# Performance work log

Measured on AMD Instinct MI355X. Metric: run time of the kernel, lower is better.

The kernel has to match this reference:

```python
import jax, jax.numpy as jnp
import numpy as np

N_NODES = 100_000
SCALAR_DIM = 64
HIDDEN = 64
ATTR_DIM = 3
N_DIH = 1_000_000
IN_DIM = SCALAR_DIM * 2 + ATTR_DIM + 2  # 133
EPS_LN = 1e-5
EPS_NORM = 1e-6


def setup_inputs() -> dict:
    key = jax.random.key(0)
    ks = jax.random.split(key, 8)
    x = jax.random.normal(ks[0], (N_NODES, SCALAR_DIM), jnp.float32)
    pos = jax.random.normal(ks[1], (N_NODES, 3), jnp.float32)
    quadra_index = jax.random.randint(ks[2], (4, N_DIH), 0, N_NODES, jnp.int32)
    quadra_attr = jax.random.normal(ks[3], (N_DIH, ATTR_DIM), jnp.float32)

    def lin(k, fi, fo):
        lim = 1.0 / np.sqrt(fi)
        return jax.random.uniform(k, (fi, fo), jnp.float32, -lim, lim)

    return dict(
        x=x, pos=pos, quadra_index=quadra_index, quadra_attr=quadra_attr,
        ln_gamma=jnp.ones((IN_DIM,), jnp.float32),
        ln_beta=jnp.zeros((IN_DIM,), jnp.float32),
        w1=lin(ks[4], IN_DIM, HIDDEN), b1=jnp.zeros((HIDDEN,), jnp.float32),
        w2=lin(ks[5], HIDDEN, HIDDEN), b2=jnp.zeros((HIDDEN,), jnp.float32),
        w3=lin(ks[6], HIDDEN, SCALAR_DIM), b3=jnp.zeros((SCALAR_DIM,), jnp.float32),
        w_out=jax.random.normal(ks[7], (SCALAR_DIM, SCALAR_DIM), jnp.float32),
    )


def _dihedral_cos_sin(pos, i, j, k, l):
    b1 = pos[j] - pos[i]
    b2 = pos[k] - pos[j]
    b3 = pos[l] - pos[k]
    n1 = jnp.cross(b1, b2)
    n2 = jnp.cross(b2, b3)
    n1 = n1 / jnp.maximum(jnp.linalg.norm(n1, axis=-1, keepdims=True), EPS_NORM)
    n2 = n2 / jnp.maximum(jnp.linalg.norm(n2, axis=-1, keepdims=True), EPS_NORM)
    cos_d = jnp.clip(jnp.sum(n1 * n2, axis=-1), -1.0, 1.0)
    b2n = b2 / jnp.maximum(jnp.linalg.norm(b2, axis=-1, keepdims=True), EPS_NORM)
    m = jnp.cross(n1, b2n)
    sin_d = jnp.sum(m * n2, axis=-1)
    return cos_d, sin_d


def _segment_mean(v, idx, n):
    s = jax.ops.segment_sum(v, idx, num_segments=n)
    c = jax.ops.segment_sum(jnp.ones((idx.shape[0], 1), v.dtype), idx, num_segments=n)
    return s / jnp.maximum(c, 1.0)


def reference(x, pos, quadra_index, quadra_attr,
              ln_gamma, ln_beta, w1, b1, w2, b2, w3, b3, w_out):
    i, j, k, l = quadra_index[0], quadra_index[1], quadra_index[2], quadra_index[3]
    x_scalar = x[:, :SCALAR_DIM]
    cos_d, sin_d = _dihedral_cos_sin(pos, i, j, k, l)
    # [num_dihedrals, 2*scalar_dim + 3 + 2]
    inp = jnp.concatenate(
        [x_scalar[i], x_scalar[l], quadra_attr, cos_d[:, None], sin_d[:, None]], axis=-1)
    # LayerNorm over last dim
    mu = jnp.mean(inp, axis=-1, keepdims=True)
    var = jnp.mean(jnp.square(inp - mu), axis=-1, keepdims=True)
    inp = (inp - mu) * jax.lax.rsqrt(var + EPS_LN) * ln_gamma + ln_beta
    # MLP with SiLU
    h = jax.nn.silu(inp @ w1 + b1)
    h = jax.nn.silu(h @ w2 + b2)
    msg = h @ w3 + b3  # [num_dihedrals, scalar_dim]
    aggr = 0.5 * (_segment_mean(msg, j, N_NODES) + _segment_mean(msg, k, N_NODES))
    # e3nn o3.Linear on scalars: fan-in normalized linear, no bias
    out = (aggr @ w_out) * (1.0 / np.sqrt(SCALAR_DIM))
    return out
```

## Files before the change

### kernel.cpp

```cpp
#include <hip/hip_runtime.h>
#include <math.h>

#define NN 100000
#define ND 1000000
#define INDIM 133
#define K1P 160
#define NCNT (2*NN)
#define SCAN_CHUNK 2048
#define NBLK_SCAN ((NCNT + SCAN_CHUNK - 1) / SCAN_CHUNK)
#define HS 72

typedef __bf16 bf16x8 __attribute__((ext_vector_type(8)));
typedef __bf16 bf16x4 __attribute__((ext_vector_type(4)));
typedef float  f32x4  __attribute__((ext_vector_type(4)));
typedef _Float16 f16;
typedef _Float16 f16x4 __attribute__((ext_vector_type(4)));

__device__ __forceinline__ f32x4 mfma_bf16(bf16x8 a, bf16x8 b, f32x4 c) {
    return __builtin_amdgcn_mfma_f32_16x16x32_bf16(a, b, c, 0, 0, 0);
}

__device__ __forceinline__ float3 f3sub(float3 a, float3 b) {
    return make_float3(a.x - b.x, a.y - b.y, a.z - b.z);
}
__device__ __forceinline__ float3 f3cross(float3 a, float3 b) {
    return make_float3(a.y * b.z - a.z * b.y, a.z * b.x - a.x * b.z, a.x * b.y - a.y * b.x);
}
__device__ __forceinline__ float f3dot(float3 a, float3 b) {
    return a.x * b.x + a.y * b.y + a.z * b.z;
}
__device__ __forceinline__ float3 f3load(const float* __restrict__ p, int idx) {
    const float* q = p + (size_t)idx * 3;
    return make_float3(q[0], q[1], q[2]);
}
__device__ __forceinline__ float fsilu(float v) {
    return v / (1.0f + __expf(-v));
}

__global__ __launch_bounds__(256) void prep_w1g(const float* __restrict__ w1,
                                                const float* __restrict__ gamma,
                                                __bf16* __restrict__ hi,
                                                __bf16* __restrict__ lo) {
    int idx = blockIdx.x * 256 + threadIdx.x;
    if (idx >= 64 * K1P) return;
    int n = idx / K1P, kp = idx - n * K1P;
    float v = (kp < INDIM) ? gamma[kp] * w1[(size_t)kp * 64 + n] : 0.0f;
    __bf16 h = (__bf16)v;
    hi[idx] = h;
    lo[idx] = (__bf16)(v - (float)h);
}

__global__ __launch_bounds__(64) void prep_lin(const float* __restrict__ w1,
                                               const float* __restrict__ b1,
                                               const float* __restrict__ gamma,
                                               const float* __restrict__ beta,
                                               float* __restrict__ c1,
                                               float* __restrict__ d1) {
    const int c = threadIdx.x;
    float sc = 0.0f, sd = 0.0f;
    for (int k = 0; k < INDIM; ++k) {
        float w = w1[(size_t)k * 64 + c];
        sc = fmaf(gamma[k], w, sc);
        sd = fmaf(beta[k], w, sd);
    }
    c1[c] = sc;
    d1[c] = sd + b1[c];
}

__global__ __launch_bounds__(256) void prep_w(const float* __restrict__ w,
                                              __bf16* __restrict__ hi,
                                              __bf16* __restrict__ lo) {
    int idx = blockIdx.x * 256 + threadIdx.x;
    if (idx >= 64 * 64) return;
    int n = idx >> 6, kp = idx & 63;
    int ko = 16 * (kp & 3) + (kp >> 2);
    float v = w[(size_t)ko * 64 + n];
    __bf16 h = (__bf16)v;
    hi[idx] = h;
    lo[idx] = (__bf16)(v - (float)h);
}

__global__ __launch_bounds__(256) void prep_w3(const float* __restrict__ w3,
                                               const float* __restrict__ b3,
                                               const float* __restrict__ wout,
                                               __bf16* __restrict__ hiT,
                                               __bf16* __restrict__ loT,
                                               float* __restrict__ b3f) {
    const int tid = threadIdx.x;
    for (int idx = tid; idx < 64 * 64; idx += 256) {
        int k = idx >> 6, c = idx & 63;
        float s = 0.0f;
        for (int q = 0; q < 64; ++q)
            s = fmaf(w3[(size_t)k * 64 + q], wout[(size_t)q * 64 + c], s);
        s *= 0.0625f;
        __bf16 h = (__bf16)s;
        int kp = 4 * (k & 15) + (k >> 4);
        hiT[(size_t)c * 64 + kp] = h;
        loT[(size_t)c * 64 + kp] = (__bf16)(s - (float)h);
    }
    if (tid < 64) {
        float s = 0.0f;
        for (int q = 0; q < 64; ++q)
            s = fmaf(b3[q], wout[(size_t)q * 64 + tid], s);
        b3f[tid] = s * 0.0625f;
    }
}

__global__ __launch_bounds__(256) void count_kernel(const int* __restrict__ qidx,
                                                    int* __restrict__ cnt) {
    int e = blockIdx.x * 256 + threadIdx.x;
    if (e < ND) {
        atomicAdd(&cnt[qidx[ND + e]], 1);
        atomicAdd(&cnt[NN + qidx[2 * ND + e]], 1);
    }
}

__global__ __launch_bounds__(256) void scan1(int* data, int* __restrict__ bsum) {
    __shared__ int lds[256];
    const int tid = threadIdx.x;
    const int base = blockIdx.x * SCAN_CHUNK + tid * 8;
    int v[8];
    int tsum = 0;
#pragma unroll
    for (int t = 0; t < 8; ++t) {
        v[t] = (base + t < NCNT) ? data[base + t] : 0;
        tsum += v[t];
    }
    lds[tid] = tsum;
    __syncthreads();
    for (int d = 1; d < 256; d <<= 1) {
        int t = 0;
        if (tid >= d) t = lds[tid - d];
        __syncthreads();
        lds[tid] += t;
        __syncthreads();
    }
    if (tid == 255) bsum[blockIdx.x] = lds[255];
    int run = lds[tid] - tsum;
#pragma unroll
    for (int t = 0; t < 8; ++t) {
        if (base + t < NCNT) data[base + t] = run;
        run += v[t];
    }
}

__global__ __launch_bounds__(128) void scan2(int* __restrict__ bsum) {
    __shared__ int lds[128];
    const int t = threadIdx.x;
    int v = (t < NBLK_SCAN) ? bsum[t] : 0;
    lds[t] = v;
    __syncthreads();
    for (int d = 1; d < 128; d <<= 1) {
        int u = (t >= d) ? lds[t - d] : 0;
        __syncthreads();
        lds[t] += u;
        __syncthreads();
    }
    if (t < NBLK_SCAN) bsum[t] = lds[t] - v;
}

__global__ __launch_bounds__(256) void scan3(int* __restrict__ off,
                                             const int* __restrict__ bsum) {
    const int base = blockIdx.x * SCAN_CHUNK + threadIdx.x * 8;
    const int add = bsum[blockIdx.x];
#pragma unroll
    for (int t = 0; t < 8; ++t) {
        int i = base + t;
        if (i < NCNT) off[i] += add;
    }
}

__global__ __launch_bounds__(256) void fill_kernel(const int* __restrict__ qidx,
                                                   int* __restrict__ off,
                                                   int* __restrict__ slot_j,
                                                   int* __restrict__ slot_k) {
    int e = blockIdx.x * 256 + threadIdx.x;
    if (e < ND) {
        slot_j[e] = atomicAdd(&off[qidx[ND + e]], 1);
        slot_k[e] = atomicAdd(&off[NN + qidx[2 * ND + e]], 1);
    }
}

__global__ __launch_bounds__(256, 3) void edge_mlp_mfma(
    const float* __restrict__ x, const float* __restrict__ pos,
    const int* __restrict__ qidx, const float* __restrict__ qattr,
    const __bf16* __restrict__ w1h, const __bf16* __restrict__ w1l,
    const float* __restrict__ c1, const float* __restrict__ d1,
    const __bf16* __restrict__ w2h, const __bf16* __restrict__ w2l, const float* __restrict__ b2,
    const __bf16* __restrict__ w3h, const __bf16* __restrict__ w3l, const float* __restrict__ b3f,
    const int* __restrict__ slot_j, const int* __restrict__ slot_k,
    f16* __restrict__ msg)
{
    __shared__ __align__(16) __bf16 hsh[4][2][16 * HS];

    const int tid = threadIdx.x;
    const int w   = tid >> 6;
    const int l   = tid & 63;
    const int m   = l & 15;
    const int kg  = l >> 4;
    const int ebase = (blockIdx.x * 4 + w) * 32;
    if (ebase >= ND) return;

    int iA[2], lA[2];
#pragma unroll
    for (int t = 0; t < 2; ++t) {
        const int e = ebase + 16 * t + m;
        iA[t] = qidx[e];
        lA[t] = qidx[3 * ND + e];
    }

    float cosd = 0.f, sind = 0.f, at0 = 0.f, at1 = 0.f, at2 = 0.f, se = 0.f, qe = 0.f;
    if (kg < 2) {
        const int e2 = ebase + 16 * kg + m;
        const int j2 = qidx[ND + e2];
        const int k2 = qidx[2 * ND + e2];
        float3 pi = f3load(pos, iA[kg]), pj = f3load(pos, j2);
        float3 pk = f3load(pos, k2), pl = f3load(pos, lA[kg]);
        float3 d1v_ = f3sub(pj, pi);
        float3 d2v_ = f3sub(pk, pj);
        float3 d3v_ = f3sub(pl, pk);
        float3 n1 = f3cross(d1v_, d2v_);
        float3 n2 = f3cross(d2v_, d3v_);
        float r1 = 1.0f / fmaxf(sqrtf(f3dot(n1, n1)), 1e-6f);
        n1.x *= r1; n1.y *= r1; n1.z *= r1;
        float r2 = 1.0f / fmaxf(sqrtf(f3dot(n2, n2)), 1e-6f);
        n2.x *= r2; n2.y *= r2; n2.z *= r2;
        cosd = fminf(fmaxf(f3dot(n1, n2), -1.0f), 1.0f);
        float rb = 1.0f / fmaxf(sqrtf(f3dot(d2v_, d2v_)), 1e-6f);
        float3 b2n = make_float3(d2v_.x * rb, d2v_.y * rb, d2v_.z * rb);
        float3 mm = f3cross(n1, b2n);
        sind = f3dot(mm, n2);
        at0 = qattr[(size_t)e2 * 3 + 0];
        at1 = qattr[(size_t)e2 * 3 + 1];
        at2 = qattr[(size_t)e2 * 3 + 2];
        se = at0 + at1 + at2 + cosd + sind;
        qe = at0 * at0 + at1 * at1 + at2 * at2 + cosd * cosd + sind * sind;
    }

    bf16x8 ah4[2], al4[2];
#pragma unroll
    for (int t = 0; t < 2; ++t) {
        const int src = m + 16 * t;
        float u4[8] = {__shfl(at0, src), __shfl(at1, src), __shfl(at2, src),
                       __shfl(cosd, src), __shfl(sind, src), 0.f, 0.f, 0.f};
        float g0 = (kg == 0) ? 1.0f : 0.0f;
#pragma unroll
        for (int j = 0; j < 8; ++j) {
            float v = u4[j] * g0;
            __bf16 h = (__bf16)v;
            ah4[t][j] = h;
            al4[t][j] = (__bf16)(v - (float)h);
        }
    }

    f32x4 acc[2][4];
#pragma unroll
    for (int t = 0; t < 2; ++t)
#pragma unroll
        for (int nt = 0; nt < 4; ++nt) acc[t][nt] = (f32x4){0.f, 0.f, 0.f, 0.f};

#pragma unroll
    for (int nt = 0; nt < 4; ++nt) {
        const size_t wb = (size_t)(16 * nt + m) * K1P + 128 + 8 * kg;
        bf16x8 bh = *(const bf16x8*)(w1h + wb);
        bf16x8 bl = *(const bf16x8*)(w1l + wb);
        acc[0][nt] = mfma_bf16(ah4[0], bh, acc[0][nt]);
        acc[0][nt] = mfma_bf16(al4[0], bh, acc[0][nt]);
        acc[0][nt] = mfma_bf16(ah4[0], bl, acc[0][nt]);
        acc[1][nt] = mfma_bf16(ah4[1], bh, acc[1][nt]);
        acc[1][nt] = mfma_bf16(al4[1], bh, acc[1][nt]);
        acc[1][nt] = mfma_bf16(ah4[1], bl, acc[1][nt]);
    }

    float st1[2] = {0.f, 0.f}, st2[2] = {0.f, 0.f};
#pragma unroll
    for (int s = 0; s < 4; ++s) {
        const int r0 = (s < 2) ? iA[0] : lA[0];
        const int r1 = (s < 2) ? iA[1] : lA[1];
        const int colo = 32 * (s & 1) + 8 * kg;
        float vv0[8], vv1[8];
        *(float4*)&vv0[0] = *(const float4*)(x + (size_t)r0 * 64 + colo);
        *(float4*)&vv0[4] = *(const float4*)(x + (size_t)r0 * 64 + colo + 4);
        *(float4*)&vv1[0] = *(const float4*)(x + (size_t)r1 * 64 + colo);
        *(float4*)&vv1[4] = *(const float4*)(x + (size_t)r1 * 64 + colo + 4);
        bf16x8 a0h, a0l, a1h, a1l;
#pragma unroll
        for (int j = 0; j < 8; ++j) {
            float v0 = vv0[j], v1 = vv1[j];
            __bf16 h0 = (__bf16)v0, h1 = (__bf16)v1;
            a0h[j] = h0; a0l[j] = (__bf16)(v0 - (float)h0);
            a1h[j] = h1; a1l[j] = (__bf16)(v1 - (float)h1);
            st1[0] += v0; st2[0] = fmaf(v0, v0, st2[0]);
            st1[1] += v1; st2[1] = fmaf(v1, v1, st2[1]);
        }
#pragma unroll
        for (int nt = 0; nt < 4; ++nt) {
            const size_t wb = (size_t)(16 * nt + m) * K1P + 32 * s + 8 * kg;
            bf16x8 bh = *(const bf16x8*)(w1h + wb);
            bf16x8 bl = *(const bf16x8*)(w1l + wb);
            acc[0][nt] = mfma_bf16(a0h, bh, acc[0][nt]);
            acc[0][nt] = mfma_bf16(a0l, bh, acc[0][nt]);
            acc[0][nt] = mfma_bf16(a0h, bl, acc[0][nt]);
            acc[1][nt] = mfma_bf16(a1h, bh, acc[1][nt]);
            acc[1][nt] = mfma_bf16(a1l, bh, acc[1][nt]);
            acc[1][nt] = mfma_bf16(a1h, bl, acc[1][nt]);
        }
    }

    float rs_[2], mn_[2];
#pragma unroll
    for (int t = 0; t < 2; ++t) {
        float s1 = st1[t], s2 = st2[t];
        s1 += __shfl_xor(s1, 16); s1 += __shfl_xor(s1, 32);
        s2 += __shfl_xor(s2, 16); s2 += __shfl_xor(s2, 32);
        const int src = m + 16 * t;
        float S = s1 + __shfl(se, src);
        float Q = s2 + __shfl(qe, src);
        float mu  = S * (1.0f / INDIM);
        float var = Q * (1.0f / INDIM) - mu * mu;
        float rsv = rsqrtf(fmaxf(var, 0.0f) + 1e-5f);
        rs_[t] = rsv;
        mn_[t] = -mu * rsv;
    }

    float c1v[4], d1v[4], b2v[4], b3v[4];
#pragma unroll
    for (int nt = 0; nt < 4; ++nt) {
        c1v[nt] = c1[16 * nt + m];
        d1v[nt] = d1[16 * nt + m];
        b2v[nt] = b2[16 * nt + m];
        b3v[nt] = b3f[16 * nt + m];
    }
#pragma unroll
    for (int t = 0; t < 2; ++t) {
        __bf16* hhw = &hsh[w][t][0];
#pragma unroll
        for (int r = 0; r < 4; ++r) {
            float rse = __shfl(rs_[t], 4 * kg + r);
            float mne = __shfl(mn_[t], 4 * kg + r);
            bf16x4 hv4;
#pragma unroll
            for (int nt = 0; nt < 4; ++nt)
                hv4[nt] = (__bf16)fsilu(fmaf(rse, acc[t][nt][r],
                                        fmaf(mne, c1v[nt], d1v[nt])));
            *(bf16x4*)(hhw + (4 * kg + r) * HS + m * 4) = hv4;
        }
    }

    bf16x8 a2h[2][2];
#pragma unroll
    for (int t = 0; t < 2; ++t)
#pragma unroll
        for (int s = 0; s < 2; ++s)
            a2h[t][s] = *(const bf16x8*)(&hsh[w][t][m * HS + 32 * s + 8 * kg]);
    f32x4 acc2[2][4];
#pragma unroll
    for (int t = 0; t < 2; ++t)
#pragma unroll
        for (int nt = 0; nt < 4; ++nt) acc2[t][nt] = (f32x4){0.f, 0.f, 0.f, 0.f};
#pragma unroll
    for (int s = 0; s < 2; ++s) {
#pragma unroll
        for (int nt = 0; nt < 4; ++nt) {
            const size_t wb = (size_t)(16 * nt + m) * 64 + 32 * s + 8 * kg;
            bf16x8 bh = *(const bf16x8*)(w2h + wb);
            bf16x8 bl = *(const bf16x8*)(w2l + wb);
            acc2[0][nt] = mfma_bf16(a2h[0][s], bh, acc2[0][nt]);
            acc2[0][nt] = mfma_bf16(a2h[0][s], bl, acc2[0][nt]);
            acc2[1][nt] = mfma_bf16(a2h[1][s], bh, acc2[1][nt]);
            acc2[1][nt] = mfma_bf16(a2h[1][s], bl, acc2[1][nt]);
        }
    }
#pragma unroll
    for (int t = 0; t < 2; ++t) {
        __bf16* hhw = &hsh[w][t][0];
#pragma unroll
        for (int r = 0; r < 4; ++r) {
            bf16x4 hv4;
#pragma unroll
            for (int nt = 0; nt < 4; ++nt)
                hv4[nt] = (__bf16)fsilu(acc2[t][nt][r] + b2v[nt]);
            *(bf16x4*)(hhw + (4 * kg + r) * HS + m * 4) = hv4;
        }
    }

    bf16x8 a3h[2][2];
#pragma unroll
    for (int t = 0; t < 2; ++t)
#pragma unroll
        for (int s = 0; s < 2; ++s)
            a3h[t][s] = *(const bf16x8*)(&hsh[w][t][m * HS + 32 * s + 8 * kg]);
    f32x4 acc3[2][4];
#pragma unroll
    for (int t = 0; t < 2; ++t)
#pragma unroll
        for (int nt = 0; nt < 4; ++nt) acc3[t][nt] = (f32x4){0.f, 0.f, 0.f, 0.f};
#pragma unroll
    for (int s = 0; s < 2; ++s) {
#pragma unroll
        for (int nt = 0; nt < 4; ++nt) {
            const size_t wb = (size_t)(16 * nt + m) * 64 + 32 * s + 8 * kg;
            bf16x8 bh = *(const bf16x8*)(w3h + wb);
            bf16x8 bl = *(const bf16x8*)(w3l + wb);
            acc3[0][nt] = mfma_bf16(a3h[0][s], bh, acc3[0][nt]);
            acc3[0][nt] = mfma_bf16(a3h[0][s], bl, acc3[0][nt]);
            acc3[1][nt] = mfma_bf16(a3h[1][s], bh, acc3[1][nt]);
            acc3[1][nt] = mfma_bf16(a3h[1][s], bl, acc3[1][nt]);
        }
    }

#pragma unroll
    for (int t = 0; t < 2; ++t) {
#pragma unroll
        for (int r = 0; r < 4; ++r) {
            f16x4 v;
#pragma unroll
            for (int nt = 0; nt < 4; ++nt)
                v[nt] = (f16)(acc3[t][nt][r] + b3v[nt]);
            const int er = ebase + 16 * t + 4 * kg + r;
            *(f16x4*)(msg + (size_t)slot_j[er] * 64 + m * 4) = v;
            *(f16x4*)(msg + (size_t)slot_k[er] * 64 + m * 4) = v;
        }
    }
}

__global__ __launch_bounds__(256) void node_out(const f16* __restrict__ msg,
                                                const int* __restrict__ off,
                                                float* __restrict__ out) {
    const int w   = threadIdx.x >> 6;
    const int l   = threadIdx.x & 63;
    const int sub = l >> 4;
    const int m16 = l & 15;
    for (int n = blockIdx.x * 4 + w; n < NN; n += gridDim.x * 4) {
        int ja = (n == 0) ? 0 : off[n - 1];
        int jb = off[n];
        int ka = off[NN + n - 1];
        int kb = off[NN + n];
        float s0 = 0.f, s1 = 0.f, s2 = 0.f, s3 = 0.f;
        float t0 = 0.f, t1 = 0.f, t2 = 0.f, t3 = 0.f;
        for (int p = ja + sub; p < jb; p += 4) {
            f16x4 v = *(const f16x4*)(msg + (size_t)p * 64 + m16 * 4);
            s0 += (float)v[0]; s1 += (float)v[1];
            s2 += (float)v[2]; s3 += (float)v[3];
        }
        for (int p = ka + sub; p < kb; p += 4) {
            f16x4 v = *(const f16x4*)(msg + (size_t)p * 64 + m16 * 4);
            t0 += (float)v[0]; t1 += (float)v[1];
            t2 += (float)v[2]; t3 += (float)v[3];
        }
        s0 += __shfl_xor(s0, 16); s0 += __shfl_xor(s0, 32);
        s1 += __shfl_xor(s1, 16); s1 += __shfl_xor(s1, 32);
        s2 += __shfl_xor(s2, 16); s2 += __shfl_xor(s2, 32);
        s3 += __shfl_xor(s3, 16); s3 += __shfl_xor(s3, 32);
        t0 += __shfl_xor(t0, 16); t0 += __shfl_xor(t0, 32);
        t1 += __shfl_xor(t1, 16); t1 += __shfl_xor(t1, 32);
        t2 += __shfl_xor(t2, 16); t2 += __shfl_xor(t2, 32);
        t3 += __shfl_xor(t3, 16); t3 += __shfl_xor(t3, 32);
        if (sub == 0) {
            float rj = 1.0f / fmaxf((float)(jb - ja), 1.0f);
            float rk = 1.0f / fmaxf((float)(kb - ka), 1.0f);
            float* o = out + (size_t)n * 64;
            o[m16]      = s0 * rj + t0 * rk;
            o[16 + m16] = s1 * rj + t1 * rk;
            o[32 + m16] = s2 * rj + t2 * rk;
            o[48 + m16] = s3 * rj + t3 * rk;
        }
    }
}


extern "C" void kernel_launch(void* const* d_in, const int* in_sizes, int n_in,
                              void* d_out, int out_size, void* d_ws, size_t ws_size,
                              hipStream_t stream) {
    (void)in_sizes; (void)n_in; (void)out_size;

    const float* x     = (const float*)d_in[0];
    const float* pos   = (const float*)d_in[1];
    const int*   qidx  = (const int*)d_in[2];
    const float* qattr = (const float*)d_in[3];
    const float* gamma = (const float*)d_in[4];
    const float* beta  = (const float*)d_in[5];
    const float* w1    = (const float*)d_in[6];
    const float* b1    = (const float*)d_in[7];
    const float* w2    = (const float*)d_in[8];
    const float* b2    = (const float*)d_in[9];
    const float* w3    = (const float*)d_in[10];
    const float* b3    = (const float*)d_in[11];
    const float* w_out = (const float*)d_in[12];
    float* out = (float*)d_out;

    size_t o = 0;
    auto alloc = [&](size_t bytes) { size_t r = o; o = (o + bytes + 255) & ~(size_t)255; return r; };
    char* W = (char*)d_ws;
    f16*    msg    = (f16*)   (W + alloc((size_t)2 * ND * 64 * sizeof(f16)));
    int*    slot_j = (int*)   (W + alloc((size_t)ND * sizeof(int)));
    int*    slot_k = (int*)   (W + alloc((size_t)ND * sizeof(int)));
    int*    off    = (int*)   (W + alloc((size_t)NCNT * sizeof(int)));
    int*    bsum   = (int*)   (W + alloc((size_t)NBLK_SCAN * sizeof(int)));
    __bf16* w1h    = (__bf16*)(W + alloc((size_t)64 * K1P * sizeof(__bf16)));
    __bf16* w1l    = (__bf16*)(W + alloc((size_t)64 * K1P * sizeof(__bf16)));
    __bf16* w2h    = (__bf16*)(W + alloc((size_t)64 * 64 * sizeof(__bf16)));
    __bf16* w2l    = (__bf16*)(W + alloc((size_t)64 * 64 * sizeof(__bf16)));
    __bf16* w3h    = (__bf16*)(W + alloc((size_t)64 * 64 * sizeof(__bf16)));
    __bf16* w3l    = (__bf16*)(W + alloc((size_t)64 * 64 * sizeof(__bf16)));
    float*  c1     = (float*) (W + alloc((size_t)64 * sizeof(float)));
    float*  d1     = (float*) (W + alloc((size_t)64 * sizeof(float)));
    float*  b3f    = (float*) (W + alloc((size_t)64 * sizeof(float)));
    if (ws_size < o) return;

    prep_w1g<<<(64 * K1P + 255) / 256, 256, 0, stream>>>(w1, gamma, w1h, w1l);
    prep_lin<<<1, 64, 0, stream>>>(w1, b1, gamma, beta, c1, d1);
    prep_w<<<16, 256, 0, stream>>>(w2, w2h, w2l);
    prep_w3<<<1, 256, 0, stream>>>(w3, b3, w_out, w3h, w3l, b3f);

    hipMemsetAsync(off, 0, (size_t)NCNT * sizeof(int), stream);
    count_kernel<<<(ND + 255) / 256, 256, 0, stream>>>(qidx, off);
    scan1<<<NBLK_SCAN, 256, 0, stream>>>(off, bsum);
    scan2<<<1, 128, 0, stream>>>(bsum);
    scan3<<<NBLK_SCAN, 256, 0, stream>>>(off, bsum);
    fill_kernel<<<(ND + 255) / 256, 256, 0, stream>>>(qidx, off, slot_j, slot_k);

    edge_mlp_mfma<<<(ND + 127) / 128, 256, 0, stream>>>(x, pos, qidx, qattr,
                                                        w1h, w1l, c1, d1,
                                                        w2h, w2l, b2, w3h, w3l, b3f,
                                                        slot_j, slot_k, msg);
    node_out<<<4096, 256, 0, stream>>>(msg, off, out);
}
```

Baseline: 595.9 us.

## Process 64 edges per wave, precompute per-node LN stats, merge prep kernels

Each wave in the edge MLP now handles 64 dihedrals instead of 32, so every loaded bf16 weight fragment is reused across four row tiles, and all four lane groups now do dihedral geometry instead of two. Per-node sum and sum-of-squares of x are precomputed once by a new kernel, so LayerNorm statistics become two float2 gathers instead of an in-kernel reduction. The four weight-prep kernels are merged into one launch. In exchange, the accumulator count doubles, which raises register pressure and may reduce occupancy under the 3-blocks-per-SM bound, and LDS use grows.

```diff
diff --git a/kernel.cpp b/kernel.cpp
--- a/kernel.cpp
+++ b/kernel.cpp
@@ -37,72 +37,77 @@
     return v / (1.0f + __expf(-v));
 }
 
-__global__ __launch_bounds__(256) void prep_w1g(const float* __restrict__ w1,
-                                                const float* __restrict__ gamma,
-                                                __bf16* __restrict__ hi,
-                                                __bf16* __restrict__ lo) {
-    int idx = blockIdx.x * 256 + threadIdx.x;
-    if (idx >= 64 * K1P) return;
-    int n = idx / K1P, kp = idx - n * K1P;
-    float v = (kp < INDIM) ? gamma[kp] * w1[(size_t)kp * 64 + n] : 0.0f;
-    __bf16 h = (__bf16)v;
-    hi[idx] = h;
-    lo[idx] = (__bf16)(v - (float)h);
-}
-
-__global__ __launch_bounds__(64) void prep_lin(const float* __restrict__ w1,
-                                               const float* __restrict__ b1,
-                                               const float* __restrict__ gamma,
-                                               const float* __restrict__ beta,
-                                               float* __restrict__ c1,
-                                               float* __restrict__ d1) {
-    const int c = threadIdx.x;
-    float sc = 0.0f, sd = 0.0f;
-    for (int k = 0; k < INDIM; ++k) {
-        float w = w1[(size_t)k * 64 + c];
-        sc = fmaf(gamma[k], w, sc);
-        sd = fmaf(beta[k], w, sd);
-    }
-    c1[c] = sc;
-    d1[c] = sd + b1[c];
-}
-
-__global__ __launch_bounds__(256) void prep_w(const float* __restrict__ w,
-                                              __bf16* __restrict__ hi,
-                                              __bf16* __restrict__ lo) {
-    int idx = blockIdx.x * 256 + threadIdx.x;
-    if (idx >= 64 * 64) return;
-    int n = idx >> 6, kp = idx & 63;
-    int ko = 16 * (kp & 3) + (kp >> 2);
-    float v = w[(size_t)ko * 64 + n];
-    __bf16 h = (__bf16)v;
-    hi[idx] = h;
-    lo[idx] = (__bf16)(v - (float)h);
-}
-
-__global__ __launch_bounds__(256) void prep_w3(const float* __restrict__ w3,
-                                               const float* __restrict__ b3,
-                                               const float* __restrict__ wout,
-                                               __bf16* __restrict__ hiT,
-                                               __bf16* __restrict__ loT,
-                                               float* __restrict__ b3f) {
-    const int tid = threadIdx.x;
-    for (int idx = tid; idx < 64 * 64; idx += 256) {
-        int k = idx >> 6, c = idx & 63;
-        float s = 0.0f;
-        for (int q = 0; q < 64; ++q)
-            s = fmaf(w3[(size_t)k * 64 + q], wout[(size_t)q * 64 + c], s);
-        s *= 0.0625f;
-        __bf16 h = (__bf16)s;
-        int kp = 4 * (k & 15) + (k >> 4);
-        hiT[(size_t)c * 64 + kp] = h;
-        loT[(size_t)c * 64 + kp] = (__bf16)(s - (float)h);
-    }
-    if (tid < 64) {
-        float s = 0.0f;
-        for (int q = 0; q < 64; ++q)
-            s = fmaf(b3[q], wout[(size_t)q * 64 + tid], s);
-        b3f[tid] = s * 0.0625f;
+__global__ __launch_bounds__(256) void prep_sq(const float* __restrict__ x,
+                                               float2* __restrict__ sq) {
+    const int n = blockIdx.x * 4 + (threadIdx.x >> 6);
+    const int c = threadIdx.x & 63;
+    float v = x[(size_t)n * 64 + c];
+    float s = v, q = v * v;
+#pragma unroll
+    for (int d = 1; d < 64; d <<= 1) {
+        s += __shfl_xor(s, d);
+        q += __shfl_xor(q, d);
+    }
+    if (c == 0) sq[n] = make_float2(s, q);
+}
+
+__global__ __launch_bounds__(256) void prep_all(
+    const float* __restrict__ w1, const float* __restrict__ b1,
+    const float* __restrict__ w2,
+    const float* __restrict__ w3, const float* __restrict__ b3,
+    const float* __restrict__ wout,
+    const float* __restrict__ gamma, const float* __restrict__ beta,
+    __bf16* __restrict__ w1h, __bf16* __restrict__ w1l,
+    float* __restrict__ c1, float* __restrict__ d1,
+    __bf16* __restrict__ w2h, __bf16* __restrict__ w2l,
+    __bf16* __restrict__ w3h, __bf16* __restrict__ w3l,
+    float* __restrict__ b3f)
+{
+    const int b = blockIdx.x, tid = threadIdx.x;
+    if (b < 40) {
+        int idx = b * 256 + tid;
+        int n = idx / K1P, kp = idx - n * K1P;
+        float v = (kp < INDIM) ? gamma[kp] * w1[(size_t)kp * 64 + n] : 0.0f;
+        __bf16 h = (__bf16)v;
+        w1h[idx] = h;
+        w1l[idx] = (__bf16)(v - (float)h);
+    } else if (b == 40) {
+        if (tid < 64) {
+            float sc = 0.0f, sd = 0.0f;
+            for (int k = 0; k < INDIM; ++k) {
+                float wv = w1[(size_t)k * 64 + tid];
+                sc = fmaf(gamma[k], wv, sc);
+                sd = fmaf(beta[k], wv, sd);
+            }
+            c1[tid] = sc;
+            d1[tid] = sd + b1[tid];
+        }
+    } else if (b < 57) {
+        int idx = (b - 41) * 256 + tid;
+        int n = idx >> 6, kp = idx & 63;
+        int ko = 16 * (kp & 3) + (kp >> 2);
+        float v = w2[(size_t)ko * 64 + n];
+        __bf16 h = (__bf16)v;
+        w2h[idx] = h;
+        w2l[idx] = (__bf16)(v - (float)h);
+    } else {
+        for (int idx = tid; idx < 64 * 64; idx += 256) {
+            int k = idx >> 6, c = idx & 63;
+            float s = 0.0f;
+            for (int q = 0; q < 64; ++q)
+                s = fmaf(w3[(size_t)k * 64 + q], wout[(size_t)q * 64 + c], s);
+            s *= 0.0625f;
+            __bf16 h = (__bf16)s;
+            int kp = 4 * (k & 15) + (k >> 4);
+            w3h[(size_t)c * 64 + kp] = h;
+            w3l[(size_t)c * 64 + kp] = (__bf16)(s - (float)h);
+        }
+        if (tid < 64) {
+            float s = 0.0f;
+            for (int q = 0; q < 64; ++q)
+                s = fmaf(b3[q], wout[(size_t)q * 64 + tid], s);
+            b3f[tid] = s * 0.0625f;
+        }
     }
 }
 
@@ -182,7 +187,8 @@
 }
 
 __global__ __launch_bounds__(256, 3) void edge_mlp_mfma(
-    const float* __restrict__ x, const float* __restrict__ pos,
+    const float* __restrict__ x, const float2* __restrict__ sq,
+    const float* __restrict__ pos,
     const int* __restrict__ qidx, const float* __restrict__ qattr,
     const __bf16* __restrict__ w1h, const __bf16* __restrict__ w1l,
     const float* __restrict__ c1, const float* __restrict__ d1,
@@ -191,31 +197,33 @@
     const int* __restrict__ slot_j, const int* __restrict__ slot_k,
     f16* __restrict__ msg)
 {
-    __shared__ __align__(16) __bf16 hsh[4][2][16 * HS];
+    __shared__ __align__(16) __bf16 hsh[4][4][16 * HS];
 
     const int tid = threadIdx.x;
     const int w   = tid >> 6;
     const int l   = tid & 63;
     const int m   = l & 15;
     const int kg  = l >> 4;
-    const int ebase = (blockIdx.x * 4 + w) * 32;
+    const int ebase = (blockIdx.x * 4 + w) * 64;
     if (ebase >= ND) return;
 
-    int iA[2], lA[2];
-#pragma unroll
-    for (int t = 0; t < 2; ++t) {
+    int iA[4], lA[4];
+#pragma unroll
+    for (int t = 0; t < 4; ++t) {
         const int e = ebase + 16 * t + m;
         iA[t] = qidx[e];
         lA[t] = qidx[3 * ND + e];
     }
 
-    float cosd = 0.f, sind = 0.f, at0 = 0.f, at1 = 0.f, at2 = 0.f, se = 0.f, qe = 0.f;
-    if (kg < 2) {
+    float cosd, sind, at0, at1, at2, se, qe;
+    {
         const int e2 = ebase + 16 * kg + m;
+        const int i2 = qidx[e2];
         const int j2 = qidx[ND + e2];
         const int k2 = qidx[2 * ND + e2];
-        float3 pi = f3load(pos, iA[kg]), pj = f3load(pos, j2);
-        float3 pk = f3load(pos, k2), pl = f3load(pos, lA[kg]);
+        const int l2 = qidx[3 * ND + e2];
+        float3 pi = f3load(pos, i2), pj = f3load(pos, j2);
+        float3 pk = f3load(pos, k2), pl = f3load(pos, l2);
         float3 d1v_ = f3sub(pj, pi);
         float3 d2v_ = f3sub(pk, pj);
         float3 d3v_ = f3sub(pl, pk);
@@ -237,9 +245,10 @@
         qe = at0 * at0 + at1 * at1 + at2 * at2 + cosd * cosd + sind * sind;
     }
 
-    bf16x8 ah4[2], al4[2];
-#pragma unroll
-    for (int t = 0; t < 2; ++t) {
+    bf16x8 ah4[4], al4[4];
+    float rs_[4], mn_[4];
+#pragma unroll
+    for (int t = 0; t < 4; ++t) {
         const int src = m + 16 * t;
         float u4[8] = {__shfl(at0, src), __shfl(at1, src), __shfl(at2, src),
                        __shfl(cosd, src), __shfl(sind, src), 0.f, 0.f, 0.f};
@@ -251,71 +260,9 @@
             ah4[t][j] = h;
             al4[t][j] = (__bf16)(v - (float)h);
         }
-    }
-
-    f32x4 acc[2][4];
-#pragma unroll
-    for (int t = 0; t < 2; ++t)
-#pragma unroll
-        for (int nt = 0; nt < 4; ++nt) acc[t][nt] = (f32x4){0.f, 0.f, 0.f, 0.f};
-
-#pragma unroll
-    for (int nt = 0; nt < 4; ++nt) {
-        const size_t wb = (size_t)(16 * nt + m) * K1P + 128 + 8 * kg;
-        bf16x8 bh = *(const bf16x8*)(w1h + wb);
-        bf16x8 bl = *(const bf16x8*)(w1l + wb);
-        acc[0][nt] = mfma_bf16(ah4[0], bh, acc[0][nt]);
-        acc[0][nt] = mfma_bf16(al4[0], bh, acc[0][nt]);
-        acc[0][nt] = mfma_bf16(ah4[0], bl, acc[0][nt]);
-        acc[1][nt] = mfma_bf16(ah4[1], bh, acc[1][nt]);
-        acc[1][nt] = mfma_bf16(al4[1], bh, acc[1][nt]);
-        acc[1][nt] = mfma_bf16(ah4[1], bl, acc[1][nt]);
-    }
-
-    float st1[2] = {0.f, 0.f}, st2[2] = {0.f, 0.f};
-#pragma unroll
-    for (int s = 0; s < 4; ++s) {
-        const int r0 = (s < 2) ? iA[0] : lA[0];
-        const int r1 = (s < 2) ? iA[1] : lA[1];
-        const int colo = 32 * (s & 1) + 8 * kg;
-        float vv0[8], vv1[8];
-        *(float4*)&vv0[0] = *(const float4*)(x + (size_t)r0 * 64 + colo);
-        *(float4*)&vv0[4] = *(const float4*)(x + (size_t)r0 * 64 + colo + 4);
-        *(float4*)&vv1[0] = *(const float4*)(x + (size_t)r1 * 64 + colo);
-        *(float4*)&vv1[4] = *(const float4*)(x + (size_t)r1 * 64 + colo + 4);
-        bf16x8 a0h, a0l, a1h, a1l;
-#pragma unroll
-        for (int j = 0; j < 8; ++j) {
-            float v0 = vv0[j], v1 = vv1[j];
-            __bf16 h0 = (__bf16)v0, h1 = (__bf16)v1;
-            a0h[j] = h0; a0l[j] = (__bf16)(v0 - (float)h0);
-            a1h[j] = h1; a1l[j] = (__bf16)(v1 - (float)h1);
-            st1[0] += v0; st2[0] = fmaf(v0, v0, st2[0]);
-            st1[1] += v1; st2[1] = fmaf(v1, v1, st2[1]);
-        }
-#pragma unroll
-        for (int nt = 0; nt < 4; ++nt) {
-            const size_t wb = (size_t)(16 * nt + m) * K1P + 32 * s + 8 * kg;
-            bf16x8 bh = *(const bf16x8*)(w1h + wb);
-            bf16x8 bl = *(const bf16x8*)(w1l + wb);
-            acc[0][nt] = mfma_bf16(a0h, bh, acc[0][nt]);
-            acc[0][nt] = mfma_bf16(a0l, bh, acc[0][nt]);
-            acc[0][nt] = mfma_bf16(a0h, bl, acc[0][nt]);
-            acc[1][nt] = mfma_bf16(a1h, bh, acc[1][nt]);
-            acc[1][nt] = mfma_bf16(a1l, bh, acc[1][nt]);
-            acc[1][nt] = mfma_bf16(a1h, bl, acc[1][nt]);
-        }
-    }
-
-    float rs_[2], mn_[2];
-#pragma unroll
-    for (int t = 0; t < 2; ++t) {
-        float s1 = st1[t], s2 = st2[t];
-        s1 += __shfl_xor(s1, 16); s1 += __shfl_xor(s1, 32);
-        s2 += __shfl_xor(s2, 16); s2 += __shfl_xor(s2, 32);
-        const int src = m + 16 * t;
-        float S = s1 + __shfl(se, src);
-        float Q = s2 + __shfl(qe, src);
+        float2 si = sq[iA[t]], sl = sq[lA[t]];
+        float S = si.x + sl.x + __shfl(se, src);
+        float Q = si.y + sl.y + __shfl(qe, src);
         float mu  = S * (1.0f / INDIM);
         float var = Q * (1.0f / INDIM) - mu * mu;
         float rsv = rsqrtf(fmaxf(var, 0.0f) + 1e-5f);
@@ -323,6 +270,57 @@
         mn_[t] = -mu * rsv;
     }
 
+    f32x4 acc[4][4];
+#pragma unroll
+    for (int t = 0; t < 4; ++t)
+#pragma unroll
+        for (int nt = 0; nt < 4; ++nt) acc[t][nt] = (f32x4){0.f, 0.f, 0.f, 0.f};
+
+#pragma unroll
+    for (int nt = 0; nt < 4; ++nt) {
+        const size_t wb = (size_t)(16 * nt + m) * K1P + 128 + 8 * kg;
+        bf16x8 bh = *(const bf16x8*)(w1h + wb);
+        bf16x8 bl = *(const bf16x8*)(w1l + wb);
+#pragma unroll
+        for (int t = 0; t < 4; ++t) {
+            acc[t][nt] = mfma_bf16(ah4[t], bh, acc[t][nt]);
+            acc[t][nt] = mfma_bf16(al4[t], bh, acc[t][nt]);
+            acc[t][nt] = mfma_bf16(ah4[t], bl, acc[t][nt]);
+        }
+    }
+
+#pragma unroll
+    for (int s = 0; s < 4; ++s) {
+        const int colo = 32 * (s & 1) + 8 * kg;
+        bf16x8 ath[4], atl[4];
+#pragma unroll
+        for (int t = 0; t < 4; ++t) {
+            const int r_ = (s < 2) ? iA[t] : lA[t];
+            float vv[8];
+            *(float4*)&vv[0] = *(const float4*)(x + (size_t)r_ * 64 + colo);
+            *(float4*)&vv[4] = *(const float4*)(x + (size_t)r_ * 64 + colo + 4);
+#pragma unroll
+            for (int j = 0; j < 8; ++j) {
+                float v = vv[j];
+                __bf16 h = (__bf16)v;
+                ath[t][j] = h;
+                atl[t][j] = (__bf16)(v - (float)h);
+            }
+        }
+#pragma unroll
+        for (int nt = 0; nt < 4; ++nt) {
+            const size_t wb = (size_t)(16 * nt + m) * K1P + 32 * s + 8 * kg;
+            bf16x8 bh = *(const bf16x8*)(w1h + wb);
+            bf16x8 bl = *(const bf16x8*)(w1l + wb);
+#pragma unroll
+            for (int t = 0; t < 4; ++t) {
+                acc[t][nt] = mfma_bf16(ath[t], bh, acc[t][nt]);
+                acc[t][nt] = mfma_bf16(atl[t], bh, acc[t][nt]);
+                acc[t][nt] = mfma_bf16(ath[t], bl, acc[t][nt]);
+            }
+        }
+    }
+
     float c1v[4], d1v[4], b2v[4], b3v[4];
 #pragma unroll
     for (int nt = 0; nt < 4; ++nt) {
@@ -332,7 +330,7 @@
         b3v[nt] = b3f[16 * nt + m];
     }
 #pragma unroll
-    for (int t = 0; t < 2; ++t) {
+    for (int t = 0; t < 4; ++t) {
         __bf16* hhw = &hsh[w][t][0];
 #pragma unroll
         for (int r = 0; r < 4; ++r) {
@@ -347,15 +345,15 @@
         }
     }
 
-    bf16x8 a2h[2][2];
-#pragma unroll
-    for (int t = 0; t < 2; ++t)
+    bf16x8 a2h[4][2];
+#pragma unroll
+    for (int t = 0; t < 4; ++t)
 #pragma unroll
         for (int s = 0; s < 2; ++s)
             a2h[t][s] = *(const bf16x8*)(&hsh[w][t][m * HS + 32 * s + 8 * kg]);
-    f32x4 acc2[2][4];
-#pragma unroll
-    for (int t = 0; t < 2; ++t)
+    f32x4 acc2[4][4];
+#pragma unroll
+    for (int t = 0; t < 4; ++t)
 #pragma unroll
         for (int nt = 0; nt < 4; ++nt) acc2[t][nt] = (f32x4){0.f, 0.f, 0.f, 0.f};
 #pragma unroll
@@ -365,14 +363,15 @@
             const size_t wb = (size_t)(16 * nt + m) * 64 + 32 * s + 8 * kg;
             bf16x8 bh = *(const bf16x8*)(w2h + wb);
             bf16x8 bl = *(const bf16x8*)(w2l + wb);
-            acc2[0][nt] = mfma_bf16(a2h[0][s], bh, acc2[0][nt]);
-            acc2[0][nt] = mfma_bf16(a2h[0][s], bl, acc2[0][nt]);
-            acc2[1][nt] = mfma_bf16(a2h[1][s], bh, acc2[1][nt]);
-            acc2[1][nt] = mfma_bf16(a2h[1][s], bl, acc2[1][nt]);
-        }
-    }
-#pragma unroll
-    for (int t = 0; t < 2; ++t) {
+#pragma unroll
+            for (int t = 0; t < 4; ++t) {
+                acc2[t][nt] = mfma_bf16(a2h[t][s], bh, acc2[t][nt]);
+                acc2[t][nt] = mfma_bf16(a2h[t][s], bl, acc2[t][nt]);
+            }
+        }
+    }
+#pragma unroll
+    for (int t = 0; t < 4; ++t) {
         __bf16* hhw = &hsh[w][t][0];
 #pragma unroll
         for (int r = 0; r < 4; ++r) {
@@ -384,15 +383,15 @@
         }
     }
 
-    bf16x8 a3h[2][2];
-#pragma unroll
-    for (int t = 0; t < 2; ++t)
+    bf16x8 a3h[4][2];
+#pragma unroll
+    for (int t = 0; t < 4; ++t)
 #pragma unroll
         for (int s = 0; s < 2; ++s)
             a3h[t][s] = *(const bf16x8*)(&hsh[w][t][m * HS + 32 * s + 8 * kg]);
-    f32x4 acc3[2][4];
-#pragma unroll
-    for (int t = 0; t < 2; ++t)
+    f32x4 acc3[4][4];
+#pragma unroll
+    for (int t = 0; t < 4; ++t)
 #pragma unroll
         for (int nt = 0; nt < 4; ++nt) acc3[t][nt] = (f32x4){0.f, 0.f, 0.f, 0.f};
 #pragma unroll
@@ -402,15 +401,16 @@
             const size_t wb = (size_t)(16 * nt + m) * 64 + 32 * s + 8 * kg;
             bf16x8 bh = *(const bf16x8*)(w3h + wb);
             bf16x8 bl = *(const bf16x8*)(w3l + wb);
-            acc3[0][nt] = mfma_bf16(a3h[0][s], bh, acc3[0][nt]);
-            acc3[0][nt] = mfma_bf16(a3h[0][s], bl, acc3[0][nt]);
-            acc3[1][nt] = mfma_bf16(a3h[1][s], bh, acc3[1][nt]);
-            acc3[1][nt] = mfma_bf16(a3h[1][s], bl, acc3[1][nt]);
-        }
-    }
-
-#pragma unroll
-    for (int t = 0; t < 2; ++t) {
+#pragma unroll
+            for (int t = 0; t < 4; ++t) {
+                acc3[t][nt] = mfma_bf16(a3h[t][s], bh, acc3[t][nt]);
+                acc3[t][nt] = mfma_bf16(a3h[t][s], bl, acc3[t][nt]);
+            }
+        }
+    }
+
+#pragma unroll
+    for (int t = 0; t < 4; ++t) {
 #pragma unroll
         for (int r = 0; r < 4; ++r) {
             f16x4 v;
@@ -497,6 +497,7 @@
     int*    slot_k = (int*)   (W + alloc((size_t)ND * sizeof(int)));
     int*    off    = (int*)   (W + alloc((size_t)NCNT * sizeof(int)));
     int*    bsum   = (int*)   (W + alloc((size_t)NBLK_SCAN * sizeof(int)));
+    float2* sqt    = (float2*)(W + alloc((size_t)NN * sizeof(float2)));
     __bf16* w1h    = (__bf16*)(W + alloc((size_t)64 * K1P * sizeof(__bf16)));
     __bf16* w1l    = (__bf16*)(W + alloc((size_t)64 * K1P * sizeof(__bf16)));
     __bf16* w2h    = (__bf16*)(W + alloc((size_t)64 * 64 * sizeof(__bf16)));
@@ -508,10 +509,9 @@
     float*  b3f    = (float*) (W + alloc((size_t)64 * sizeof(float)));
     if (ws_size < o) return;
 
-    prep_w1g<<<(64 * K1P + 255) / 256, 256, 0, stream>>>(w1, gamma, w1h, w1l);
-    prep_lin<<<1, 64, 0, stream>>>(w1, b1, gamma, beta, c1, d1);
-    prep_w<<<16, 256, 0, stream>>>(w2, w2h, w2l);
-    prep_w3<<<1, 256, 0, stream>>>(w3, b3, w_out, w3h, w3l, b3f);
+    prep_sq<<<NN / 4, 256, 0, stream>>>(x, sqt);
+    prep_all<<<58, 256, 0, stream>>>(w1, b1, w2, w3, b3, w_out, gamma, beta,
+                                     w1h, w1l, c1, d1, w2h, w2l, w3h, w3l, b3f);
 
     hipMemsetAsync(off, 0, (size_t)NCNT * sizeof(int), stream);
     count_kernel<<<(ND + 255) / 256, 256, 0, stream>>>(qidx, off);
@@ -520,9 +520,9 @@
     scan3<<<NBLK_SCAN, 256, 0, stream>>>(off, bsum);
     fill_kernel<<<(ND + 255) / 256, 256, 0, stream>>>(qidx, off, slot_j, slot_k);
 
-    edge_mlp_mfma<<<(ND + 127) / 128, 256, 0, stream>>>(x, pos, qidx, qattr,
-                                                        w1h, w1l, c1, d1,
-                                                        w2h, w2l, b2, w3h, w3l, b3f,
-                                                        slot_j, slot_k, msg);
+    edge_mlp_mfma<<<(ND / 64 + 3) / 4, 256, 0, stream>>>(x, sqt, pos, qidx, qattr,
+                                                         w1h, w1l, c1, d1,
+                                                         w2h, w2l, b2, w3h, w3l, b3f,
+                                                         slot_j, slot_k, msg);
     node_out<<<4096, 256, 0, stream>>>(msg, off, out);
 }
```

Result: faster. 541.4 us (-9.1%).
